# Performance work log

Hardware: AMD Instinct MI355X
Metric: run time of the kernel (lower is better)

## Reference

```python
import jax, jax.numpy as jnp
import numpy as np

B, N, H, HC = 2, 10000, 8, 32   # batch, tokens (= u*v*h*w), heads, head_dim
UV, D = 25, 5                   # angular views u*v, number of disparity hypotheses
HW = N // UV                    # spatial positions per view
L = D * N                       # gathered segment length = disp * uv * hw


def setup_inputs() -> dict:
    key = jax.random.key(0)
    k1, k2, k3, k4, k5 = jax.random.split(key, 5)
    qkv = jax.random.normal(k1, (3, B, N, H, HC), dtype=jnp.float32)
    attn_idx = jax.random.randint(k2, (L,), 0, N)          # gather/scatter token index
    attn_inv = jax.random.permutation(k3, L)               # permutation (disp-major <-> token-major)
    attn_idx2 = jax.random.permutation(k4, L)
    mask = jax.random.uniform(k5, (N, UV * D)) > 0.3       # valid (uv2, disp) pairs per token
    mask = mask.at[:, 0].set(True)                         # avoid fully-masked rows
    disp_map = jnp.linspace(-2.0, 2.0, UV * D).astype(jnp.float32)
    return {"qkv": qkv, "disp_map": disp_map, "mask": mask,
            "attn_idx": attn_idx, "attn_idx2": attn_idx2, "attn_inv": attn_inv,
            "disp_size": D, "uv": UV}


def reference(qkv, disp_map, mask, attn_idx, attn_idx2, attn_inv, disp_size, uv):
    _, b, n, h, hc = qkv.shape
    L = attn_idx.shape[0]
    hw = L // (disp_size * uv)
    uvhw = uv * hw  # == n here

    seg = jnp.take(qkv, attn_idx, axis=2)                  # [3, b, L, h, hc]
    q, k, v = seg[0], seg[1], seg[2]
    # 'b (disp uv hw) head hc -> b disp hw head uv hc'
    q = q.reshape(b, disp_size, uv, hw, h, hc).transpose(0, 1, 3, 4, 2, 5)
    k = k.reshape(b, disp_size, uv, hw, h, hc).transpose(0, 1, 3, 4, 2, 5)
    v = v.reshape(b, disp_size, uv, hw, h, hc).transpose(0, 1, 3, 4, 2, 5)

    scale = np.float32(1.0 / np.sqrt(hc))
    aw = jnp.einsum('bdwhuc,bdwhvc->bdwhuv', q, k) * scale  # b disp hw head uv1 uv2
    # 'b disp hw head uv1 uv2 -> b (disp uv1 hw) head uv2'
    aw = aw.transpose(0, 1, 4, 2, 3, 5).reshape(b, L, h, uv)
    aw = aw[:, attn_inv]
    # 'b (disp uv1hw) head uv2 -> b uv1hw head (uv2 disp)'
    aw = aw.reshape(b, disp_size, uvhw, h, uv).transpose(0, 2, 3, 4, 1).reshape(b, uvhw, h, uv * disp_size)

    bias = jnp.where(mask, 0.0, -jnp.inf).astype(aw.dtype)  # [uvhw, uv*disp]
    aw = jax.nn.softmax(aw + bias[None, :, None, :], axis=-1)

    disp = jnp.sum(aw * disp_map[None, None, None, :], axis=-1)  # [b, uvhw, h]

    # 'b uv1hw head (uv2 disp) -> b (disp uv1hw) head uv2'
    aw = aw.reshape(b, uvhw, h, uv, disp_size).transpose(0, 4, 1, 2, 3).reshape(b, L, h, uv)
    aw = aw[:, attn_idx2]
    # 'b (disp uv1 hw) head uv2 -> b disp hw head uv1 uv2'
    aw = aw.reshape(b, disp_size, uv, hw, h, uv).transpose(0, 1, 3, 4, 2, 5)

    out = jnp.einsum('bdwhuv,bdwhvc->bdwhuc', aw, v)        # b disp hw head uv hc
    # 'b disp hw head uv hc -> b (disp uv hw) (head hc)'
    out = out.transpose(0, 1, 4, 2, 3, 5).reshape(b, L, h * hc)

    attn_out = jnp.zeros((b, n, h * hc), dtype=qkv.dtype).at[:, attn_idx].add(out)
    return attn_out, disp
```

## Files before the change

### kernel.cpp

```cpp
#include <hip/hip_runtime.h>
#include <math.h>

#define B 2
#define N 10000
#define H 8
#define HC 32
#define UV 25
#define DD 5
#define HW 400
#define L 50000
#define UVHW 10000
#define MCOL 125

static __device__ __forceinline__ size_t qkv_off(int s, int b, int n, int h) {
    return ((((size_t)s * B + b) * N + n) * H + h) * HC;
}

__global__ __launch_bounds__(256) void k_qk(const float* __restrict__ qkv,
                                            const int* __restrict__ attn_idx,
                                            float* __restrict__ aw2) {
    const float SCALE = 0.17677669529663687f;
    int bid = blockIdx.x;
    int b = bid / (DD * HW);
    int rem = bid % (DD * HW);
    int d = rem / HW, w = rem % HW;
    int t = threadIdx.x;

    __shared__ int idx[UV];
    __shared__ float qs[UV][HC + 1];
    __shared__ float ks[UV][HC + 1];

    if (t < UV) idx[t] = attn_idx[(d * UV + t) * HW + w];
    __syncthreads();

    for (int h = 0; h < H; ++h) {
        for (int e = t; e < UV * HC; e += 256) {
            int u = e / HC, c = e % HC;
            qs[u][c] = qkv[qkv_off(0, b, idx[u], h) + c];
            ks[u][c] = qkv[qkv_off(1, b, idx[u], h) + c];
        }
        __syncthreads();
        for (int e = t; e < UV * UV; e += 256) {
            int u = e / UV, v = e % UV;
            float acc = 0.f;
#pragma unroll
            for (int c = 0; c < HC; ++c) acc += qs[u][c] * ks[v][c];
            int lu = (d * UV + u) * HW + w;
            aw2[(((size_t)b * L + lu) * H + h) * UV + v] = acc * SCALE;
        }
        __syncthreads();
    }
}

__global__ __launch_bounds__(256) void k_softmax(const float* __restrict__ aw2,
                                                 const int* __restrict__ attn_inv,
                                                 const void* __restrict__ maskbuf,
                                                 const float* __restrict__ disp_map,
                                                 float* __restrict__ p_ws,
                                                 float* __restrict__ disp) {
    int bid = blockIdx.x;
    int b = bid / UVHW, j = bid % UVHW;
    int t = threadIdx.x;
    int h = t >> 5, lane = t & 31;

    __shared__ int linv[DD];
    __shared__ int s_flag;

    if (t == 0) s_flag = 0;
    if (t < DD) linv[t] = attn_inv[t * UVHW + j];
    __syncthreads();
    const unsigned char* mb = (const unsigned char*)maskbuf;
    if (t < 64) {
        if (mb[4 * t + 1] | mb[4 * t + 2] | mb[4 * t + 3]) s_flag = 1;
    }
    __syncthreads();
    bool isbyte = (s_flag != 0);
    const int* mw = (const int*)maskbuf;

    float vals[4];
    float m = -INFINITY;
#pragma unroll
    for (int kk = 0; kk < 4; ++kk) {
        int e = lane + kk * 32;
        float x = -INFINITY;
        if (e < MCOL) {
            int v = e / DD, d2 = e % DD;
            int l = linv[d2];
            float raw = aw2[(((size_t)b * L + l) * H + h) * UV + v];
            int mv = isbyte ? (int)mb[(size_t)j * MCOL + e] : mw[(size_t)j * MCOL + e];
            x = mv ? raw : -INFINITY;
        }
        vals[kk] = x;
        m = fmaxf(m, x);
    }
#pragma unroll
    for (int s = 16; s >= 1; s >>= 1) m = fmaxf(m, __shfl_xor(m, s, 32));
    float sum = 0.f;
#pragma unroll
    for (int kk = 0; kk < 4; ++kk) {
        float pe = expf(vals[kk] - m);
        vals[kk] = pe;
        sum += pe;
    }
#pragma unroll
    for (int s = 16; s >= 1; s >>= 1) sum += __shfl_xor(sum, s, 32);
    float inv = 1.0f / sum;
    float dacc = 0.f;
    size_t pb = (((size_t)b * UVHW + j) * H + h) * MCOL;
#pragma unroll
    for (int kk = 0; kk < 4; ++kk) {
        int e = lane + kk * 32;
        if (e < MCOL) {
            float pe = vals[kk] * inv;
            p_ws[pb + e] = pe;
            dacc += pe * disp_map[e];
        }
    }
#pragma unroll
    for (int s = 16; s >= 1; s >>= 1) dacc += __shfl_xor(dacc, s, 32);
    if (lane == 0) disp[((size_t)b * UVHW + j) * H + h] = dacc;
}

__global__ __launch_bounds__(256) void k_pv(const float* __restrict__ qkv,
                                            const int* __restrict__ attn_idx,
                                            const int* __restrict__ attn_idx2,
                                            const float* __restrict__ p_ws,
                                            float* __restrict__ attn_out) {
    int bid = blockIdx.x;
    int b = bid / (DD * HW * H);
    int rem = bid % (DD * HW * H);
    int d = rem / (HW * H);
    int rem2 = rem % (HW * H);
    int w = rem2 / H, h = rem2 % H;
    int t = threadIdx.x;

    __shared__ int idxv[UV];
    __shared__ int lj[UV];
    __shared__ int ld2[UV];
    __shared__ float aw7[UV][UV + 1];
    __shared__ float vs[UV][HC + 1];

    if (t < UV) {
        int m = (d * UV + t) * HW + w;
        idxv[t] = attn_idx[m];
        int lm = attn_idx2[m];
        lj[t] = lm % UVHW;
        ld2[t] = lm / UVHW;
    }
    __syncthreads();

    for (int e = t; e < UV * UV; e += 256) {
        int u = e / UV, v = e % UV;
        aw7[u][v] = p_ws[(((size_t)b * UVHW + lj[u]) * H + h) * MCOL + v * DD + ld2[u]];
    }
    const float* vbase = qkv + (size_t)2 * B * N * H * HC;
    for (int e = t; e < UV * HC; e += 256) {
        int v = e / HC, c = e % HC;
        vs[v][c] = vbase[(((size_t)b * N + idxv[v]) * H + h) * HC + c];
    }
    __syncthreads();

    for (int e = t; e < UV * HC; e += 256) {
        int u = e / HC, c = e % HC;
        float acc = 0.f;
#pragma unroll
        for (int v = 0; v < UV; ++v) acc += aw7[u][v] * vs[v][c];
        atomicAdd(&attn_out[((size_t)b * N + idxv[u]) * (H * HC) + h * HC + c], acc);
    }
}

extern "C" void kernel_launch(void* const* d_in, const int* in_sizes, int n_in,
                              void* d_out, int out_size, void* d_ws, size_t ws_size,
                              hipStream_t stream) {
    const float* qkv      = (const float*)d_in[0];
    const float* disp_map = (const float*)d_in[1];
    const void*  mask     = d_in[2];
    const int*   attn_idx  = (const int*)d_in[3];
    const int*   attn_idx2 = (const int*)d_in[4];
    const int*   attn_inv  = (const int*)d_in[5];

    float* attn_out = (float*)d_out;
    float* disp     = (float*)d_out + (size_t)B * N * H * HC;

    float* aw2  = (float*)d_ws;
    float* p_ws = aw2 + (size_t)B * L * H * UV;

    hipMemsetAsync(d_out, 0, (size_t)B * N * H * HC * sizeof(float), stream);

    k_qk<<<B * DD * HW, 256, 0, stream>>>(qkv, attn_idx, aw2);
    k_softmax<<<B * UVHW, 256, 0, stream>>>(aw2, attn_inv, mask, disp_map, p_ws, disp);
    k_pv<<<B * DD * HW * H, 256, 0, stream>>>(qkv, attn_idx, attn_idx2, p_ws, attn_out);
}
```

Measured before the change: 253.1 us.

## Scatter softmax output through inverted permutation so PV reads contiguous rows

Adds a kernel that inverts the attn_idx2 permutation. The softmax kernel now stages probabilities in shared memory and scatters them in the layout the PV kernel consumes, so PV reads contiguous 25-float rows instead of strided gathers. The QK and PV staging loads also switch to float4 vector loads. Correctness relies on attn_idx2 being a permutation, and the change costs an extra kernel launch, a larger workspace and scattered writes in softmax.

After: 242.6 us. -4.1%, faster.

```diff
diff --git a/kernel.cpp b/kernel.cpp
--- a/kernel.cpp
+++ b/kernel.cpp
@@ -16,6 +16,12 @@
     return ((((size_t)s * B + b) * N + n) * H + h) * HC;
 }
 
+__global__ __launch_bounds__(256) void k_inv(const int* __restrict__ attn_idx2,
+                                             int* __restrict__ inv2) {
+    int i = blockIdx.x * 256 + threadIdx.x;
+    if (i < L) inv2[attn_idx2[i]] = i;
+}
+
 __global__ __launch_bounds__(256) void k_qk(const float* __restrict__ qkv,
                                             const int* __restrict__ attn_idx,
                                             float* __restrict__ aw2) {
@@ -34,10 +40,14 @@
     __syncthreads();
 
     for (int h = 0; h < H; ++h) {
-        for (int e = t; e < UV * HC; e += 256) {
-            int u = e / HC, c = e % HC;
-            qs[u][c] = qkv[qkv_off(0, b, idx[u], h) + c];
-            ks[u][c] = qkv[qkv_off(1, b, idx[u], h) + c];
+        for (int e0 = t; e0 < 2 * UV * (HC / 4); e0 += 256) {
+            int which = e0 / (UV * (HC / 4));
+            int e = e0 % (UV * (HC / 4));
+            int u = e / (HC / 4), c4 = e % (HC / 4);
+            const float4* src = (const float4*)(qkv + qkv_off(which, b, idx[u], h)) + c4;
+            float4 val = *src;
+            float* dst = (which == 0 ? &qs[u][c4 * 4] : &ks[u][c4 * 4]);
+            dst[0] = val.x; dst[1] = val.y; dst[2] = val.z; dst[3] = val.w;
         }
         __syncthreads();
         for (int e = t; e < UV * UV; e += 256) {
@@ -54,9 +64,10 @@
 
 __global__ __launch_bounds__(256) void k_softmax(const float* __restrict__ aw2,
                                                  const int* __restrict__ attn_inv,
+                                                 const int* __restrict__ inv2,
                                                  const void* __restrict__ maskbuf,
                                                  const float* __restrict__ disp_map,
-                                                 float* __restrict__ p_ws,
+                                                 float* __restrict__ p3,
                                                  float* __restrict__ disp) {
     int bid = blockIdx.x;
     int b = bid / UVHW, j = bid % UVHW;
@@ -64,10 +75,15 @@
     int h = t >> 5, lane = t & 31;
 
     __shared__ int linv[DD];
+    __shared__ int minv2[DD];
     __shared__ int s_flag;
+    __shared__ float sp[DD][H][UV];
 
     if (t == 0) s_flag = 0;
-    if (t < DD) linv[t] = attn_inv[t * UVHW + j];
+    if (t < DD) {
+        linv[t] = attn_inv[t * UVHW + j];
+        minv2[t] = inv2[t * UVHW + j];
+    }
     __syncthreads();
     const unsigned char* mb = (const unsigned char*)maskbuf;
     if (t < 64) {
@@ -106,25 +122,31 @@
     for (int s = 16; s >= 1; s >>= 1) sum += __shfl_xor(sum, s, 32);
     float inv = 1.0f / sum;
     float dacc = 0.f;
-    size_t pb = (((size_t)b * UVHW + j) * H + h) * MCOL;
 #pragma unroll
     for (int kk = 0; kk < 4; ++kk) {
         int e = lane + kk * 32;
         if (e < MCOL) {
             float pe = vals[kk] * inv;
-            p_ws[pb + e] = pe;
+            int v = e / DD, d2 = e % DD;
+            sp[d2][h][v] = pe;
             dacc += pe * disp_map[e];
         }
     }
 #pragma unroll
     for (int s = 16; s >= 1; s >>= 1) dacc += __shfl_xor(dacc, s, 32);
     if (lane == 0) disp[((size_t)b * UVHW + j) * H + h] = dacc;
+    __syncthreads();
+    for (int e2 = t; e2 < DD * H * UV; e2 += 256) {
+        int d2 = e2 / (H * UV);
+        int r = e2 % (H * UV);
+        int h2 = r / UV, v2 = r % UV;
+        p3[(((size_t)b * L + minv2[d2]) * H + h2) * UV + v2] = sp[d2][h2][v2];
+    }
 }
 
 __global__ __launch_bounds__(256) void k_pv(const float* __restrict__ qkv,
                                             const int* __restrict__ attn_idx,
-                                            const int* __restrict__ attn_idx2,
-                                            const float* __restrict__ p_ws,
+                                            const float* __restrict__ p3,
                                             float* __restrict__ attn_out) {
     int bid = blockIdx.x;
     int b = bid / (DD * HW * H);
@@ -135,28 +157,24 @@
     int t = threadIdx.x;
 
     __shared__ int idxv[UV];
-    __shared__ int lj[UV];
-    __shared__ int ld2[UV];
     __shared__ float aw7[UV][UV + 1];
     __shared__ float vs[UV][HC + 1];
 
-    if (t < UV) {
-        int m = (d * UV + t) * HW + w;
-        idxv[t] = attn_idx[m];
-        int lm = attn_idx2[m];
-        lj[t] = lm % UVHW;
-        ld2[t] = lm / UVHW;
-    }
+    if (t < UV) idxv[t] = attn_idx[(d * UV + t) * HW + w];
     __syncthreads();
 
     for (int e = t; e < UV * UV; e += 256) {
         int u = e / UV, v = e % UV;
-        aw7[u][v] = p_ws[(((size_t)b * UVHW + lj[u]) * H + h) * MCOL + v * DD + ld2[u]];
+        int m = (d * UV + u) * HW + w;
+        aw7[u][v] = p3[(((size_t)b * L + m) * H + h) * UV + v];
     }
     const float* vbase = qkv + (size_t)2 * B * N * H * HC;
-    for (int e = t; e < UV * HC; e += 256) {
-        int v = e / HC, c = e % HC;
-        vs[v][c] = vbase[(((size_t)b * N + idxv[v]) * H + h) * HC + c];
+    if (t < UV * (HC / 4)) {
+        int v = t / (HC / 4), c4 = t % (HC / 4);
+        const float4* src = (const float4*)(vbase + (((size_t)b * N + idxv[v]) * H + h) * HC) + c4;
+        float4 val = *src;
+        vs[v][c4 * 4 + 0] = val.x; vs[v][c4 * 4 + 1] = val.y;
+        vs[v][c4 * 4 + 2] = val.z; vs[v][c4 * 4 + 3] = val.w;
     }
     __syncthreads();
 
@@ -182,12 +200,14 @@
     float* attn_out = (float*)d_out;
     float* disp     = (float*)d_out + (size_t)B * N * H * HC;
 
-    float* aw2  = (float*)d_ws;
-    float* p_ws = aw2 + (size_t)B * L * H * UV;
+    float* aw2 = (float*)d_ws;
+    float* p3  = aw2 + (size_t)B * L * H * UV;
+    int*   inv2 = (int*)(p3 + (size_t)B * L * H * UV);
 
     hipMemsetAsync(d_out, 0, (size_t)B * N * H * HC * sizeof(float), stream);
 
+    k_inv<<<(L + 255) / 256, 256, 0, stream>>>(attn_idx2, inv2);
     k_qk<<<B * DD * HW, 256, 0, stream>>>(qkv, attn_idx, aw2);
-    k_softmax<<<B * UVHW, 256, 0, stream>>>(aw2, attn_inv, mask, disp_map, p_ws, disp);
-    k_pv<<<B * DD * HW * H, 256, 0, stream>>>(qkv, attn_idx, attn_idx2, p_ws, attn_out);
-}
+    k_softmax<<<B * UVHW, 256, 0, stream>>>(aw2, attn_inv, inv2, mask, disp_map, p3, disp);
+    k_pv<<<B * DD * HW * H, 256, 0, stream>>>(qkv, attn_idx, p3, attn_out);
+}
```
